# Optimization experiments

Hardware: AMD Instinct MI355X
Metric: run time of the kernel (lower is better)

## Reference

```python
import jax, jax.numpy as jnp
import numpy as np

N_IN, N_HID, N_OUT = 200, 256, 2
BN_EPS = 1e-5


def _mlp(x, W1, b1, W2, b2):
    # two-layer MLP with ELU activations (dropout prob = 0.0 -> omitted)
    h = jax.nn.elu(x @ W1 + b1)
    return jax.nn.elu(h @ W2 + b2)


def _batch_norm(x, gamma, beta):
    # torch BatchNorm1d in training mode over flattened (B*E) rows, biased variance
    m = x.mean(axis=(0, 1))
    v = x.var(axis=(0, 1))
    return (x - m) * jax.lax.rsqrt(v + BN_EPS) * gamma + beta


def setup_inputs() -> dict:
    key = jax.random.key(0)
    ks = jax.random.split(key, 12)
    B, N, T, D = 32, 100, 50, 4
    inputs = jax.random.normal(ks[0], (B, N, T, D), dtype=jnp.float32)
    # one-hot receiver/sender matrices over all N*(N-1) ordered off-diagonal pairs
    idx = np.array([(i, j) for i in range(N) for j in range(N) if i != j])
    eye = np.eye(N, dtype=np.float32)
    rel_rec = jnp.asarray(eye[idx[:, 0]])   # [E, N]
    rel_send = jnp.asarray(eye[idx[:, 1]])  # [E, N]

    def lin(k, fi, fo):  # xavier_normal weight
        std = float(np.sqrt(2.0 / (fi + fo)))
        return jax.random.normal(k, (fi, fo), dtype=jnp.float32) * std

    b = lambda n: jnp.full((n,), 0.1, dtype=jnp.float32)
    return dict(
        inputs=inputs, rel_rec=rel_rec, rel_send=rel_send,
        mlp1_W1=lin(ks[1], N_IN, N_HID), mlp1_b1=b(N_HID),
        mlp1_W2=lin(ks[2], N_HID, N_HID), mlp1_b2=b(N_HID),
        mlp2_W1=lin(ks[3], 2 * N_HID, N_HID), mlp2_b1=b(N_HID),
        mlp2_W2=lin(ks[4], N_HID, N_HID), mlp2_b2=b(N_HID),
        mlp3_W1=lin(ks[5], N_HID, N_HID), mlp3_b1=b(N_HID),
        mlp3_W2=lin(ks[6], N_HID, N_HID), mlp3_b2=b(N_HID),
        mlp4_W1=lin(ks[7], 3 * N_HID, N_HID), mlp4_b1=b(N_HID),
        mlp4_W2=lin(ks[8], N_HID, N_HID), mlp4_b2=b(N_HID),
        mlp4_bn_gamma=jnp.ones((N_HID,), jnp.float32),
        mlp4_bn_beta=jnp.zeros((N_HID,), jnp.float32),
        fc_W=lin(ks[9], N_HID, N_OUT), fc_b=b(N_OUT),
    )


def reference(inputs, rel_rec, rel_send,
              mlp1_W1, mlp1_b1, mlp1_W2, mlp1_b2,
              mlp2_W1, mlp2_b1, mlp2_W2, mlp2_b2,
              mlp3_W1, mlp3_b1, mlp3_W2, mlp3_b2,
              mlp4_W1, mlp4_b1, mlp4_W2, mlp4_b2,
              mlp4_bn_gamma, mlp4_bn_beta, fc_W, fc_b):
    B, N = inputs.shape[0], inputs.shape[1]
    x = inputs.reshape(B, N, -1)                       # [B, N, T*D]
    x = _mlp(x, mlp1_W1, mlp1_b1, mlp1_W2, mlp1_b2)     # [B, N, H]

    def node2edge(h):
        recv = jnp.einsum('en,bnh->beh', rel_rec, h)
        send = jnp.einsum('en,bnh->beh', rel_send, h)
        return jnp.concatenate([send, recv], axis=2)    # [B, E, 2H]

    x = node2edge(x)
    x = _mlp(x, mlp2_W1, mlp2_b1, mlp2_W2, mlp2_b2)     # [B, E, H]
    x_skip = x
    # factor=True branch
    incoming = jnp.einsum('en,beh->bnh', rel_rec, x) / x.shape[1]  # edge2node, /N per code
    x = _mlp(incoming, mlp3_W1, mlp3_b1, mlp3_W2, mlp3_b2)
    x = node2edge(x)                                    # [B, E, 2H]
    x = jnp.concatenate([x, x_skip], axis=2)            # [B, E, 3H]
    x = _mlp(x, mlp4_W1, mlp4_b1, mlp4_W2, mlp4_b2)
    x = _batch_norm(x, mlp4_bn_gamma, mlp4_bn_beta)
    return x @ fc_W + fc_b                              # [B, E, n_out]
```

## Files before the change

### kernel.cpp

```cpp
#include <hip/hip_runtime.h>
#include <math.h>


typedef unsigned short ushort_t;
typedef __bf16 bf16x8 __attribute__((ext_vector_type(8)));
typedef float  f32x4  __attribute__((ext_vector_type(4)));

#define E_EDGES 9900
#define NNODE   100
#define HID     256
#define M_BIG   316800
#define M_SMALL 3200
#define NBLK2   (M_BIG / 128)

__device__ __forceinline__ float bf2f(ushort_t u) {
    union { unsigned int i; float f; } v; v.i = ((unsigned int)u) << 16; return v.f;
}
__device__ __forceinline__ ushort_t f2bf(float f) {
    union { __bf16 h; ushort_t u; } v; v.h = (__bf16)f; return v.u;
}
__device__ __forceinline__ float elu_f(float x) {
    return x > 0.f ? x : (__expf(x) - 1.f);
}

__global__ __launch_bounds__(256)
void wcvt_all(const float* __restrict__ s0, const float* __restrict__ s1,
              const float* __restrict__ s2, const float* __restrict__ s3,
              const float* __restrict__ s4, const float* __restrict__ s5,
              const float* __restrict__ s6, const float* __restrict__ s7,
              ushort_t* d0, ushort_t* d1, ushort_t* d2, ushort_t* d3,
              ushort_t* d4, ushort_t* d5, ushort_t* d6, ushort_t* d7)
{
    int bid = blockIdx.x;
    const float* S; ushort_t* D; int Kd, Kr, t;
    if      (bid < 16)  { S = s0; D = d0; Kd = 256; Kr = 200; t = bid; }
    else if (bid < 32)  { S = s1; D = d1; Kd = 256; Kr = 256; t = bid - 16; }
    else if (bid < 64)  { S = s2; D = d2; Kd = 512; Kr = 512; t = bid - 32; }
    else if (bid < 80)  { S = s3; D = d3; Kd = 256; Kr = 256; t = bid - 64; }
    else if (bid < 96)  { S = s4; D = d4; Kd = 256; Kr = 256; t = bid - 80; }
    else if (bid < 112) { S = s5; D = d5; Kd = 256; Kr = 256; t = bid - 96; }
    else if (bid < 160) { S = s6; D = d6; Kd = 768; Kr = 768; t = bid - 112; }
    else                { S = s7; D = d7; Kd = 256; Kr = 256; t = bid - 160; }
    int k0 = (t >> 2) * 64, c0 = (t & 3) * 64;
    __shared__ float Sh[64][65];
    int tid = threadIdx.x;
    #pragma unroll
    for (int i = 0; i < 16; ++i) {
        int idx = tid + i * 256;
        int kk = idx >> 6, cc = idx & 63;
        Sh[kk][cc] = (k0 + kk < Kr) ? S[(size_t)(k0 + kk) * 256 + c0 + cc] : 0.f;
    }
    __syncthreads();
    int col = tid & 63;
    int kb  = (tid >> 6) * 16;
    ushort_t* dst = D + (size_t)(c0 + col) * Kd + k0 + kb;
    #pragma unroll
    for (int jj = 0; jj < 4; ++jj) {
        ushort4 u;
        u.x = f2bf(Sh[kb + 4 * jj + 0][col]);
        u.y = f2bf(Sh[kb + 4 * jj + 1][col]);
        u.z = f2bf(Sh[kb + 4 * jj + 2][col]);
        u.w = f2bf(Sh[kb + 4 * jj + 3][col]);
        *(ushort4*)(dst + 4 * jj) = u;
    }
}

__device__ __forceinline__ void gemm32(const ushort_t S[32][264],
                                       const ushort_t* __restrict__ WT,
                                       int wstr, int kcn,
                                       int w, int ln15, int klane,
                                       f32x4 acc[2][4])
{
    #pragma unroll
    for (int r = 0; r < 2; ++r)
        #pragma unroll
        for (int c = 0; c < 4; ++c)
            acc[r][c][0] = acc[r][c][1] = acc[r][c][2] = acc[r][c][3] = 0.f;
    int wch[4];
    #pragma unroll
    for (int c = 0; c < 4; ++c) wch[c] = (w * 64 + 16 * c + ln15) * wstr;
    bf16x8 wf0[4];
    #pragma unroll
    for (int c = 0; c < 4; ++c)
        wf0[c] = *(const bf16x8*)(WT + wch[c] + klane);
    for (int kc = 0; kc < kcn; ++kc) {
        bf16x8 wf1[4];
        if (kc + 1 < kcn) {
            #pragma unroll
            for (int c = 0; c < 4; ++c)
                wf1[c] = *(const bf16x8*)(WT + wch[c] + (kc + 1) * 32 + klane);
        }
        bf16x8 af[2];
        #pragma unroll
        for (int r = 0; r < 2; ++r)
            af[r] = *(const bf16x8*)&S[16 * r + ln15][kc * 32 + klane];
        #pragma unroll
        for (int r = 0; r < 2; ++r)
            #pragma unroll
            for (int c = 0; c < 4; ++c)
                acc[r][c] = __builtin_amdgcn_mfma_f32_16x16x32_bf16(wf0[c], af[r], acc[r][c], 0, 0, 0);
        #pragma unroll
        for (int c = 0; c < 4; ++c) wf0[c] = wf1[c];
    }
}

__device__ __forceinline__ void park32(ushort_t D[32][264], f32x4 acc[2][4],
                                       const float* __restrict__ bias,
                                       int act, int w, int ln15, int q)
{
    #pragma unroll
    for (int c = 0; c < 4; ++c) {
        float4 bv = bias ? *(const float4*)&bias[w * 64 + 16 * c + 4 * q]
                         : make_float4(0.f, 0.f, 0.f, 0.f);
        #pragma unroll
        for (int r = 0; r < 2; ++r) {
            float o0 = acc[r][c][0] + bv.x;
            float o1 = acc[r][c][1] + bv.y;
            float o2 = acc[r][c][2] + bv.z;
            float o3 = acc[r][c][3] + bv.w;
            if (act) { o0 = elu_f(o0); o1 = elu_f(o1); o2 = elu_f(o2); o3 = elu_f(o3); }
            ushort4 u;
            u.x = f2bf(o0); u.y = f2bf(o1); u.z = f2bf(o2); u.w = f2bf(o3);
            *(ushort4*)&D[16 * r + ln15][w * 64 + 16 * c + 4 * q] = u;
        }
    }
}

__global__ __launch_bounds__(256, 4)
void mlp_pq(const float* __restrict__ Xf, const float* __restrict__ Xf2,
            int Kreal, int kcN, float xscale,
            const ushort_t* __restrict__ W1T, const float* __restrict__ b1,
            const ushort_t* __restrict__ W2T, const float* __restrict__ b2,
            const ushort_t* __restrict__ WPT, int wsPQ,
            const float* __restrict__ bP, ushort_t* __restrict__ Pout,
            const ushort_t* __restrict__ WQT, ushort_t* __restrict__ Qout)
{
    __shared__ ushort_t Abuf[32][264];
    __shared__ ushort_t Bbuf[32][264];
    const int tid = threadIdx.x;
    const int w = tid >> 6;
    const int l = tid & 63;
    const int ln15 = l & 15;
    const int q = l >> 4;
    const int klane = 8 * q;
    const int Rbase = blockIdx.x * 32;

    {
        int row = tid >> 3, seg = tid & 7;
        if (seg < kcN) {
            ushort_t tmp[32];
            const float* src  = Xf + (size_t)(Rbase + row) * Kreal + seg * 32;
            const float* src2 = Xf2 ? Xf2 + (size_t)(Rbase + row) * Kreal + seg * 32
                                    : (const float*)nullptr;
            #pragma unroll
            for (int u = 0; u < 32; ++u) {
                float a = 0.f;
                if (seg * 32 + u < Kreal) {
                    a = src[u];
                    if (Xf2) a += src2[u];
                }
                tmp[u] = f2bf(a * xscale);
            }
            #pragma unroll
            for (int u = 0; u < 4; ++u)
                *(uint4*)&Abuf[row][seg * 32 + u * 8] = *(uint4*)&tmp[u * 8];
        }
    }
    __syncthreads();

    f32x4 acc[2][4];
    gemm32(Abuf, W1T, 256, kcN, w, ln15, klane, acc);
    park32(Bbuf, acc, b1, 1, w, ln15, q);
    __syncthreads();
    gemm32(Bbuf, W2T, 256, 8, w, ln15, klane, acc);
    park32(Abuf, acc, b2, 1, w, ln15, q);
    __syncthreads();
    gemm32(Abuf, WPT, wsPQ, 8, w, ln15, klane, acc);
    park32(Bbuf, acc, bP, 0, w, ln15, q);
    __syncthreads();
    f32x4 acq[2][4];
    gemm32(Abuf, WQT, wsPQ, 8, w, ln15, klane, acq);
    #pragma unroll
    for (int m = 0; m < 4; ++m) {
        int ch = tid + m * 256;
        int row = ch >> 5;
        int o = (ch & 31) * 8;
        *(uint4*)&Pout[(size_t)(Rbase + row) * 256 + o] = *(const uint4*)&Bbuf[row][o];
    }
    __syncthreads();
    park32(Bbuf, acq, nullptr, 0, w, ln15, q);
    __syncthreads();
    #pragma unroll
    for (int m = 0; m < 4; ++m) {
        int ch = tid + m * 256;
        int row = ch >> 5;
        int o = (ch & 31) * 8;
        *(uint4*)&Qout[(size_t)(Rbase + row) * 256 + o] = *(const uint4*)&Bbuf[row][o];
    }
}

__device__ __forceinline__ void gemm128cs(const ushort_t As[128][264],
                                          const ushort_t* __restrict__ WT,
                                          int wstr, int w, int ln15, int klane,
                                          f32x4 acc[8][2])
{
    #pragma unroll
    for (int r = 0; r < 8; ++r)
        #pragma unroll
        for (int c = 0; c < 2; ++c)
            acc[r][c][0] = acc[r][c][1] = acc[r][c][2] = acc[r][c][3] = 0.f;
    int wch[2];
    #pragma unroll
    for (int c = 0; c < 2; ++c) wch[c] = (w * 32 + 16 * c + ln15) * wstr;
    bf16x8 wf0[2];
    #pragma unroll
    for (int c = 0; c < 2; ++c)
        wf0[c] = *(const bf16x8*)(WT + wch[c] + klane);
    #pragma unroll
    for (int kc = 0; kc < 8; ++kc) {
        bf16x8 wf1[2];
        if (kc < 7) {
            #pragma unroll
            for (int c = 0; c < 2; ++c)
                wf1[c] = *(const bf16x8*)(WT + wch[c] + (kc + 1) * 32 + klane);
        }
        #pragma unroll
        for (int g = 0; g < 2; ++g) {
            bf16x8 af[4];
            #pragma unroll
            for (int r = 0; r < 4; ++r)
                af[r] = *(const bf16x8*)&As[16 * (4 * g + r) + ln15][kc * 32 + klane];
            #pragma unroll
            for (int r = 0; r < 4; ++r)
                #pragma unroll
                for (int c = 0; c < 2; ++c)
                    acc[4 * g + r][c] = __builtin_amdgcn_mfma_f32_16x16x32_bf16(wf0[c], af[r], acc[4 * g + r][c], 0, 0, 0);
        }
        #pragma unroll
        for (int c = 0; c < 2; ++c) wf0[c] = wf1[c];
    }
}

__global__ __launch_bounds__(512, 4)
void edge_mlp2(const ushort_t* __restrict__ Pb, const ushort_t* __restrict__ Qb,
               const ushort_t* __restrict__ W2T,
               const float* __restrict__ b2,
               ushort_t* __restrict__ Y,
               float* __restrict__ part0, float* __restrict__ part1)
{
    __shared__ ushort_t As[128][264];
    const int tid = threadIdx.x;
    const int w = tid >> 6;
    const int l = tid & 63;
    const int ln15 = l & 15;
    const int q = l >> 4;
    const int klane = 8 * q;
    const int Rbase = blockIdx.x * 128;

    {
        int row = tid >> 2;
        int R = Rbase + row;
        int b = R / E_EDGES;
        int e = R - b * E_EDGES;
        int i = e / 99;
        int k = e - 99 * i;
        int j = k + (k >= i ? 1 : 0);
        const ushort_t* prow = Pb + (size_t)(b * NNODE + j) * HID;
        const ushort_t* qrow = Qb + (size_t)(b * NNODE + i) * HID;
        int off = (tid & 3) * 8;
        uint4 pv[8], qv[8];
        #pragma unroll
        for (int u = 0; u < 8; ++u) {
            int o = off + u * 32;
            pv[u] = *(const uint4*)(prow + o);
            qv[u] = *(const uint4*)(qrow + o);
        }
        #pragma unroll
        for (int u = 0; u < 8; ++u) {
            int o = off + u * 32;
            union { uint4 v; ushort_t s[8]; } pu, qu, hu;
            pu.v = pv[u]; qu.v = qv[u];
            #pragma unroll
            for (int x = 0; x < 8; ++x)
                hu.s[x] = f2bf(elu_f(bf2f(pu.s[x]) + bf2f(qu.s[x])));
            *(uint4*)&As[row][o] = hu.v;
        }
    }
    __syncthreads();

    f32x4 acc[8][2];
    gemm128cs(As, W2T, 256, w, ln15, klane, acc);
    __syncthreads();

    #pragma unroll
    for (int c = 0; c < 2; ++c) {
        float4 bv = *(const float4*)&b2[w * 32 + 16 * c + 4 * q];
        #pragma unroll
        for (int r = 0; r < 8; ++r) {
            ushort4 u;
            u.x = f2bf(elu_f(acc[r][c][0] + bv.x));
            u.y = f2bf(elu_f(acc[r][c][1] + bv.y));
            u.z = f2bf(elu_f(acc[r][c][2] + bv.z));
            u.w = f2bf(elu_f(acc[r][c][3] + bv.w));
            *(ushort4*)&As[16 * r + ln15][w * 32 + 16 * c + 4 * q] = u;
        }
    }
    __syncthreads();

    #pragma unroll
    for (int m = 0; m < 8; ++m) {
        int ch = tid + m * 512;
        int row = ch >> 5;
        int o = (ch & 31) * 8;
        *(uint4*)&Y[((size_t)(Rbase + row)) * 256 + o] = *(const uint4*)&As[row][o];
    }

    if (tid < 64) {
        int c4 = tid * 4;
        int bn = Rbase / 99;
        int off0 = Rbase - bn * 99;
        int left = 99 - off0;
        int first = 1;
        float s[4] = {0.f, 0.f, 0.f, 0.f};
        for (int r = 0; r < 128; ++r) {
            union { ushort4 v; ushort_t e4[4]; } u;
            u.v = *(const ushort4*)&As[r][c4];
            #pragma unroll
            for (int g = 0; g < 4; ++g) s[g] += bf2f(u.e4[g]);
            if (--left == 0) {
                float* dst = (first && off0 != 0) ? part1 : part0;
                #pragma unroll
                for (int g = 0; g < 4; ++g) {
                    dst[(size_t)bn * 256 + c4 + g] = s[g];
                    s[g] = 0.f;
                }
                ++bn; left = 99; first = 0;
            }
        }
        if (left != 99) {
            float* dst = (first && off0 != 0) ? part1 : part0;
            #pragma unroll
            for (int g = 0; g < 4; ++g)
                dst[(size_t)bn * 256 + c4 + g] = s[g];
        }
    }
}

__global__ __launch_bounds__(512, 4)
void edge_mlp4(const ushort_t* __restrict__ Pb, const ushort_t* __restrict__ Qb,
               const ushort_t* __restrict__ X2,
               const ushort_t* __restrict__ WaT, int wsA,
               const ushort_t* __restrict__ WbT, int wsB,
               const float* __restrict__ b2,
               ushort_t* __restrict__ Y, ushort_t* __restrict__ pstat)
{
    __shared__ ushort_t As[128][264];
    __shared__ float Sc[4][512];
    const int tid = threadIdx.x;
    const int w = tid >> 6;
    const int l = tid & 63;
    const int ln15 = l & 15;
    const int q = l >> 4;
    const int klane = 8 * q;
    const int Rbase = blockIdx.x * 128;

    {
        int row = tid >> 2;
        const ushort_t* xrow = X2 + (size_t)(Rbase + row) * 256;
        int off = (tid & 3) * 8;
        uint4 xv[8];
        #pragma unroll
        for (int u = 0; u < 8; ++u) xv[u] = *(const uint4*)(xrow + off + u * 32);
        #pragma unroll
        for (int u = 0; u < 8; ++u) *(uint4*)&As[row][off + u * 32] = xv[u];
    }

    int oP[8], oQ[8];
    #pragma unroll
    for (int r = 0; r < 8; ++r) {
        int R = Rbase + 16 * r + ln15;
        int b = R / E_EDGES;
        int e = R - b * E_EDGES;
        int i = e / 99;
        int k = e - 99 * i;
        int j = k + (k >= i ? 1 : 0);
        oP[r] = (b * NNODE + j) * HID;
        oQ[r] = (b * NNODE + i) * HID;
    }
    __syncthreads();

    f32x4 acc[8][2];
    gemm128cs(As, WaT, wsA, w, ln15, klane, acc);
    __syncthreads();

    #pragma unroll
    for (int c = 0; c < 2; ++c) {
        int ch = w * 32 + 16 * c + 4 * q;
        ushort4 pv[8], qv[8];
        #pragma unroll
        for (int r = 0; r < 8; ++r) {
            pv[r] = *(const ushort4*)(Pb + oP[r] + ch);
            qv[r] = *(const ushort4*)(Qb + oQ[r] + ch);
        }
        #pragma unroll
        for (int r = 0; r < 8; ++r) {
            union { ushort4 v; ushort_t s[4]; } pu, qu;
            pu.v = pv[r]; qu.v = qv[r];
            ushort4 u;
            u.x = f2bf(elu_f(acc[r][c][0] + bf2f(pu.s[0]) + bf2f(qu.s[0])));
            u.y = f2bf(elu_f(acc[r][c][1] + bf2f(pu.s[1]) + bf2f(qu.s[1])));
            u.z = f2bf(elu_f(acc[r][c][2] + bf2f(pu.s[2]) + bf2f(qu.s[2])));
            u.w = f2bf(elu_f(acc[r][c][3] + bf2f(pu.s[3]) + bf2f(qu.s[3])));
            *(ushort4*)&As[16 * r + ln15][ch] = u;
        }
    }
    __syncthreads();

    gemm128cs(As, WbT, wsB, w, ln15, klane, acc);
    __syncthreads();

    #pragma unroll
    for (int c = 0; c < 2; ++c) {
        float4 bv = *(const float4*)&b2[w * 32 + 16 * c + 4 * q];
        #pragma unroll
        for (int r = 0; r < 8; ++r) {
            ushort4 u;
            u.x = f2bf(elu_f(acc[r][c][0] + bv.x));
            u.y = f2bf(elu_f(acc[r][c][1] + bv.y));
            u.z = f2bf(elu_f(acc[r][c][2] + bv.z));
            u.w = f2bf(elu_f(acc[r][c][3] + bv.w));
            *(ushort4*)&As[16 * r + ln15][w * 32 + 16 * c + 4 * q] = u;
        }
    }
    __syncthreads();

    #pragma unroll
    for (int m = 0; m < 8; ++m) {
        int ch = tid + m * 512;
        int row = ch >> 5;
        int o = (ch & 31) * 8;
        *(uint4*)&Y[((size_t)(Rbase + row)) * 256 + o] = *(const uint4*)&As[row][o];
    }

    if (w < 4) {
        int c4 = l * 4;
        float s[4] = {0.f, 0.f, 0.f, 0.f};
        float qq[4] = {0.f, 0.f, 0.f, 0.f};
        for (int r = w * 32; r < w * 32 + 32; ++r) {
            union { ushort4 v; ushort_t e4[4]; } u;
            u.v = *(const ushort4*)&As[r][c4];
            #pragma unroll
            for (int g = 0; g < 4; ++g) {
                float v = bf2f(u.e4[g]);
                s[g] += v;
                qq[g] = fmaf(v, v, qq[g]);
            }
        }
        #pragma unroll
        for (int g = 0; g < 4; ++g) {
            Sc[w][c4 + g]       = s[g];
            Sc[w][256 + c4 + g] = qq[g];
        }
    }
    __syncthreads();
    {
        float v = Sc[0][tid] + Sc[1][tid] + Sc[2][tid] + Sc[3][tid];
        pstat[(size_t)blockIdx.x * 512 + tid] = f2bf(v);
    }
}

__global__ __launch_bounds__(256)
void reduce_stats(const ushort_t* __restrict__ pstat, float* __restrict__ stats)
{
    int c = threadIdx.x;
    float s = 0.f, q = 0.f;
    for (int b = blockIdx.x; b < NBLK2; b += 64) {
        size_t base = (size_t)b * 512;
        s += bf2f(pstat[base + c]);
        q += bf2f(pstat[base + 256 + c]);
    }
    atomicAdd(&stats[c], s);
    atomicAdd(&stats[256 + c], q);
}

__global__ __launch_bounds__(256)
void fold_kernel(const float* __restrict__ stats,
                 const float* __restrict__ gamma, const float* __restrict__ beta,
                 const float* __restrict__ fcW, const float* __restrict__ fcb,
                 float* __restrict__ fold)
{
    __shared__ float red0[256], red1[256];
    int c = threadIdx.x;
    float mean  = stats[c] * (1.f / M_BIG);
    float var   = stats[256 + c] * (1.f / M_BIG) - mean * mean;
    float inv   = rsqrtf(var + 1e-5f);
    float scale = inv * gamma[c];
    float sh    = beta[c] - mean * scale;
    float w0 = fcW[c * 2 + 0], w1 = fcW[c * 2 + 1];
    fold[c * 2 + 0] = scale * w0;
    fold[c * 2 + 1] = scale * w1;
    red0[c] = sh * w0;
    red1[c] = sh * w1;
    __syncthreads();
    for (int off = 128; off > 0; off >>= 1) {
        if (c < off) { red0[c] += red0[c + off]; red1[c] += red1[c + off]; }
        __syncthreads();
    }
    if (c == 0) {
        fold[512] = red0[0] + fcb[0];
        fold[513] = red1[0] + fcb[1];
    }
}

__global__ __launch_bounds__(256)
void final_kernel(const ushort_t* __restrict__ x4, const float* __restrict__ fold,
                  float* __restrict__ out)
{
    int tid  = threadIdx.x;
    int l32  = tid & 31;
    int g    = tid >> 5;
    int R = blockIdx.x * 8 + g;
    int c0 = l32 * 8;
    union { uint4 qv; ushort_t s[8]; } u;
    u.qv = *(const uint4*)(x4 + (size_t)R * 256 + c0);
    float a0 = 0.f, a1 = 0.f;
    #pragma unroll
    for (int j = 0; j < 8; ++j) {
        float v = bf2f(u.s[j]);
        a0 = fmaf(v, fold[(c0 + j) * 2 + 0], a0);
        a1 = fmaf(v, fold[(c0 + j) * 2 + 1], a1);
    }
    #pragma unroll
    for (int off = 16; off > 0; off >>= 1) {
        a0 += __shfl_down(a0, off);
        a1 += __shfl_down(a1, off);
    }
    if (l32 == 0) {
        out[(size_t)R * 2 + 0] = a0 + fold[512];
        out[(size_t)R * 2 + 1] = a1 + fold[513];
    }
}

extern "C" void kernel_launch(void* const* d_in, const int* in_sizes, int n_in,
                              void* d_out, int out_size, void* d_ws, size_t ws_size,
                              hipStream_t stream)
{
    (void)in_sizes; (void)n_in; (void)out_size; (void)ws_size;

    const float* inputs = (const float*)d_in[0];
    const float* m1W1 = (const float*)d_in[3];
    const float* m1b1 = (const float*)d_in[4];
    const float* m1W2 = (const float*)d_in[5];
    const float* m1b2 = (const float*)d_in[6];
    const float* m2W1 = (const float*)d_in[7];
    const float* m2b1 = (const float*)d_in[8];
    const float* m2W2 = (const float*)d_in[9];
    const float* m2b2 = (const float*)d_in[10];
    const float* m3W1 = (const float*)d_in[11];
    const float* m3b1 = (const float*)d_in[12];
    const float* m3W2 = (const float*)d_in[13];
    const float* m3b2 = (const float*)d_in[14];
    const float* m4W1 = (const float*)d_in[15];
    const float* m4b1 = (const float*)d_in[16];
    const float* m4W2 = (const float*)d_in[17];
    const float* m4b2 = (const float*)d_in[18];
    const float* gamma = (const float*)d_in[19];
    const float* beta  = (const float*)d_in[20];
    const float* fcW   = (const float*)d_in[21];
    const float* fcb   = (const float*)d_in[22];
    float* out = (float*)d_out;

    char* ws = (char*)d_ws;
    const size_t BIGB = (size_t)M_BIG * 256 * 2;
    const size_t HB   = (size_t)M_SMALL * 256 * 2;
    const size_t SM4  = (size_t)M_SMALL * 256 * 4;
    ushort_t* bigX     = (ushort_t*)ws;
    ushort_t* pstat    = (ushort_t*)(ws + BIGB);
    float*    part1    = (float*)(ws + BIGB);
    float*    part0    = (float*)(ws + BIGB + 2 * HB);
    ushort_t* Pbuf     = (ushort_t*)(ws + BIGB + 2 * HB + SM4);
    ushort_t* Qbuf     = (ushort_t*)(ws + BIGB + 3 * HB + SM4);
    float*    stats    = (float*)(ws + BIGB + 4 * HB + SM4);
    float*    fold     = stats + 512;
    ushort_t* w1t      = (ushort_t*)(ws + BIGB + 4 * HB + SM4 + 8192);
    ushort_t* w1bt     = w1t  + 256 * 256;
    ushort_t* w2pt     = w1bt + 256 * 256;
    ushort_t* w2t      = w2pt + 256 * 512;
    ushort_t* w3at     = w2t  + 256 * 256;
    ushort_t* w3bt     = w3at + 256 * 256;
    ushort_t* w4pt     = w3bt + 256 * 256;
    ushort_t* w4bt     = w4pt + 256 * 768;

    hipMemsetAsync(stats, 0, 2048, stream);
    hipMemsetAsync(part1, 0, SM4, stream);

    dim3 blk(256);
    dim3 blk512(512);
    wcvt_all<<<176, blk, 0, stream>>>(m1W1, m1W2, m2W1, m2W2, m3W1, m3W2, m4W1, m4W2,
                                      w1t, w1bt, w2pt, w2t, w3at, w3bt, w4pt, w4bt);
    mlp_pq<<<100, blk, 0, stream>>>(inputs, nullptr, 200, 7, 1.f,
                                    w1t, m1b1, w1bt, m1b2,
                                    w2pt, 512, m2b1, Pbuf,
                                    w2pt + 256, Qbuf);
    edge_mlp2<<<NBLK2, blk512, 0, stream>>>(Pbuf, Qbuf, w2t, m2b2, bigX, part0, part1);
    mlp_pq<<<100, blk, 0, stream>>>(part0, part1, 256, 8, 1.f / 9900.f,
                                    w3at, m3b1, w3bt, m3b2,
                                    w4pt, 768, m4b1, Pbuf,
                                    w4pt + 256, Qbuf);
    edge_mlp4<<<NBLK2, blk512, 0, stream>>>(Pbuf, Qbuf, bigX,
                                            w4pt + 512, 768, w4bt, 256,
                                            m4b2, bigX, pstat);
    reduce_stats<<<64, blk, 0, stream>>>(pstat, stats);
    fold_kernel<<<1, blk, 0, stream>>>(stats, gamma, beta, fcW, fcb, fold);
    final_kernel<<<M_BIG / 8, blk, 0, stream>>>(bigX, fold, out);
}
```

Before: 471.5 us.

## Fuse column stats into GEMM epilogue and prefetch weights and gathers before barriers

Per-column sums (edge2node partial sums and batch-norm sum/sumsq) are now accumulated in registers during the ELU epilogue and reduced with wave shuffles. This replaces the serial LDS re-read done by a subset of threads and removes a shared scratch buffer and a barrier. Each GEMM's first weight fragment and the P/Q gather loads are also issued before the preceding barrier, so global latency overlaps with LDS work. The cost is higher register pressure, and the stats are summed from fp32 values instead of bf16-rounded ones, which slightly changes numerics.

```diff
diff --git a/kernel.cpp b/kernel.cpp
--- a/kernel.cpp
+++ b/kernel.cpp
@@ -199,10 +199,19 @@
     }
 }
 
+__device__ __forceinline__ void wf0_load(const ushort_t* __restrict__ WT,
+                                         int wstr, int w, int ln15, int klane,
+                                         bf16x8 wf0[2])
+{
+    #pragma unroll
+    for (int c = 0; c < 2; ++c)
+        wf0[c] = *(const bf16x8*)(WT + (w * 32 + 16 * c + ln15) * wstr + klane);
+}
+
 __device__ __forceinline__ void gemm128cs(const ushort_t As[128][264],
                                           const ushort_t* __restrict__ WT,
                                           int wstr, int w, int ln15, int klane,
-                                          f32x4 acc[8][2])
+                                          bf16x8 wf0[2], f32x4 acc[8][2])
 {
     #pragma unroll
     for (int r = 0; r < 8; ++r)
@@ -212,10 +221,6 @@
     int wch[2];
     #pragma unroll
     for (int c = 0; c < 2; ++c) wch[c] = (w * 32 + 16 * c + ln15) * wstr;
-    bf16x8 wf0[2];
-    #pragma unroll
-    for (int c = 0; c < 2; ++c)
-        wf0[c] = *(const bf16x8*)(WT + wch[c] + klane);
     #pragma unroll
     for (int kc = 0; kc < 8; ++kc) {
         bf16x8 wf1[2];
@@ -286,23 +291,56 @@
             *(uint4*)&As[row][o] = hu.v;
         }
     }
+    bf16x8 wf0[2];
+    wf0_load(W2T, 256, w, ln15, klane, wf0);
     __syncthreads();
 
     f32x4 acc[8][2];
-    gemm128cs(As, W2T, 256, w, ln15, klane, acc);
-    __syncthreads();
+    gemm128cs(As, W2T, 256, w, ln15, klane, wf0, acc);
+    __syncthreads();
+
+    const int g0   = Rbase / 99;
+    const int off0 = Rbase - g0 * 99;
+    const int t1   = 99 - off0;
+    const int t2   = t1 + 99;
+    float sA[8], sB[8], sC[8];
+    #pragma unroll
+    for (int j = 0; j < 8; ++j) { sA[j] = sB[j] = sC[j] = 0.f; }
 
     #pragma unroll
     for (int c = 0; c < 2; ++c) {
         float4 bv = *(const float4*)&b2[w * 32 + 16 * c + 4 * q];
         #pragma unroll
         for (int r = 0; r < 8; ++r) {
+            int row = 16 * r + ln15;
+            float o0 = elu_f(acc[r][c][0] + bv.x);
+            float o1 = elu_f(acc[r][c][1] + bv.y);
+            float o2 = elu_f(acc[r][c][2] + bv.z);
+            float o3 = elu_f(acc[r][c][3] + bv.w);
+            sA[c * 4 + 0] += o0; sA[c * 4 + 1] += o1;
+            sA[c * 4 + 2] += o2; sA[c * 4 + 3] += o3;
+            float m1 = (row >= t1) ? 1.f : 0.f;
+            float m2 = (row >= t2) ? 1.f : 0.f;
+            sB[c * 4 + 0] = fmaf(m1, o0, sB[c * 4 + 0]);
+            sB[c * 4 + 1] = fmaf(m1, o1, sB[c * 4 + 1]);
+            sB[c * 4 + 2] = fmaf(m1, o2, sB[c * 4 + 2]);
+            sB[c * 4 + 3] = fmaf(m1, o3, sB[c * 4 + 3]);
+            sC[c * 4 + 0] = fmaf(m2, o0, sC[c * 4 + 0]);
+            sC[c * 4 + 1] = fmaf(m2, o1, sC[c * 4 + 1]);
+            sC[c * 4 + 2] = fmaf(m2, o2, sC[c * 4 + 2]);
+            sC[c * 4 + 3] = fmaf(m2, o3, sC[c * 4 + 3]);
             ushort4 u;
-            u.x = f2bf(elu_f(acc[r][c][0] + bv.x));
-            u.y = f2bf(elu_f(acc[r][c][1] + bv.y));
-            u.z = f2bf(elu_f(acc[r][c][2] + bv.z));
-            u.w = f2bf(elu_f(acc[r][c][3] + bv.w));
-            *(ushort4*)&As[16 * r + ln15][w * 32 + 16 * c + 4 * q] = u;
+            u.x = f2bf(o0); u.y = f2bf(o1); u.z = f2bf(o2); u.w = f2bf(o3);
+            *(ushort4*)&As[row][w * 32 + 16 * c + 4 * q] = u;
+        }
+    }
+    #pragma unroll
+    for (int m = 1; m <= 8; m <<= 1) {
+        #pragma unroll
+        for (int j = 0; j < 8; ++j) {
+            sA[j] += __shfl_xor(sA[j], m);
+            sB[j] += __shfl_xor(sB[j], m);
+            sC[j] += __shfl_xor(sC[j], m);
         }
     }
     __syncthreads();
@@ -315,33 +353,26 @@
         *(uint4*)&Y[((size_t)(Rbase + row)) * 256 + o] = *(const uint4*)&As[row][o];
     }
 
-    if (tid < 64) {
-        int c4 = tid * 4;
-        int bn = Rbase / 99;
-        int off0 = Rbase - bn * 99;
-        int left = 99 - off0;
-        int first = 1;
-        float s[4] = {0.f, 0.f, 0.f, 0.f};
-        for (int r = 0; r < 128; ++r) {
-            union { ushort4 v; ushort_t e4[4]; } u;
-            u.v = *(const ushort4*)&As[r][c4];
-            #pragma unroll
-            for (int g = 0; g < 4; ++g) s[g] += bf2f(u.e4[g]);
-            if (--left == 0) {
-                float* dst = (first && off0 != 0) ? part1 : part0;
-                #pragma unroll
-                for (int g = 0; g < 4; ++g) {
-                    dst[(size_t)bn * 256 + c4 + g] = s[g];
-                    s[g] = 0.f;
-                }
-                ++bn; left = 99; first = 0;
-            }
-        }
-        if (left != 99) {
-            float* dst = (first && off0 != 0) ? part1 : part0;
-            #pragma unroll
-            for (int g = 0; g < 4; ++g)
-                dst[(size_t)bn * 256 + c4 + g] = s[g];
+    if (ln15 == 0) {
+        float* d0 = (off0 != 0) ? part1 : part0;
+        #pragma unroll
+        for (int c = 0; c < 2; ++c) {
+            int col = w * 32 + 16 * c + 4 * q;
+            float4 v0, v1, v2;
+            v0.x = sA[c * 4 + 0] - sB[c * 4 + 0];
+            v0.y = sA[c * 4 + 1] - sB[c * 4 + 1];
+            v0.z = sA[c * 4 + 2] - sB[c * 4 + 2];
+            v0.w = sA[c * 4 + 3] - sB[c * 4 + 3];
+            v1.x = sB[c * 4 + 0] - sC[c * 4 + 0];
+            v1.y = sB[c * 4 + 1] - sC[c * 4 + 1];
+            v1.z = sB[c * 4 + 2] - sC[c * 4 + 2];
+            v1.w = sB[c * 4 + 3] - sC[c * 4 + 3];
+            v2.x = sC[c * 4 + 0]; v2.y = sC[c * 4 + 1];
+            v2.z = sC[c * 4 + 2]; v2.w = sC[c * 4 + 3];
+            *(float4*)&d0[(size_t)g0 * 256 + col] = v0;
+            *(float4*)&part0[(size_t)(g0 + 1) * 256 + col] = v1;
+            if (t2 < 128)
+                *(float4*)&part0[(size_t)(g0 + 2) * 256 + col] = v2;
         }
     }
 }
@@ -355,7 +386,6 @@
                ushort_t* __restrict__ Y, ushort_t* __restrict__ pstat)
 {
     __shared__ ushort_t As[128][264];
-    __shared__ float Sc[4][512];
     const int tid = threadIdx.x;
     const int w = tid >> 6;
     const int l = tid & 63;
@@ -387,49 +417,87 @@
         oP[r] = (b * NNODE + j) * HID;
         oQ[r] = (b * NNODE + i) * HID;
     }
+
+    const int ch0 = w * 32 + 4 * q;
+    ushort4 pv0[8], qv0[8];
+    #pragma unroll
+    for (int r = 0; r < 8; ++r) {
+        pv0[r] = *(const ushort4*)(Pb + oP[r] + ch0);
+        qv0[r] = *(const ushort4*)(Qb + oQ[r] + ch0);
+    }
+    bf16x8 wfa[2];
+    wf0_load(WaT, wsA, w, ln15, klane, wfa);
     __syncthreads();
 
     f32x4 acc[8][2];
-    gemm128cs(As, WaT, wsA, w, ln15, klane, acc);
-    __syncthreads();
-
-    #pragma unroll
-    for (int c = 0; c < 2; ++c) {
-        int ch = w * 32 + 16 * c + 4 * q;
-        ushort4 pv[8], qv[8];
-        #pragma unroll
-        for (int r = 0; r < 8; ++r) {
-            pv[r] = *(const ushort4*)(Pb + oP[r] + ch);
-            qv[r] = *(const ushort4*)(Qb + oQ[r] + ch);
-        }
-        #pragma unroll
-        for (int r = 0; r < 8; ++r) {
-            union { ushort4 v; ushort_t s[4]; } pu, qu;
-            pu.v = pv[r]; qu.v = qv[r];
-            ushort4 u;
-            u.x = f2bf(elu_f(acc[r][c][0] + bf2f(pu.s[0]) + bf2f(qu.s[0])));
-            u.y = f2bf(elu_f(acc[r][c][1] + bf2f(pu.s[1]) + bf2f(qu.s[1])));
-            u.z = f2bf(elu_f(acc[r][c][2] + bf2f(pu.s[2]) + bf2f(qu.s[2])));
-            u.w = f2bf(elu_f(acc[r][c][3] + bf2f(pu.s[3]) + bf2f(qu.s[3])));
-            *(ushort4*)&As[16 * r + ln15][ch] = u;
-        }
-    }
-    __syncthreads();
-
-    gemm128cs(As, WbT, wsB, w, ln15, klane, acc);
-    __syncthreads();
-
+    gemm128cs(As, WaT, wsA, w, ln15, klane, wfa, acc);
+    bf16x8 wfb[2];
+    wf0_load(WbT, wsB, w, ln15, klane, wfb);
+    __syncthreads();
+
+    const int ch1 = ch0 + 16;
+    ushort4 pv1[8], qv1[8];
+    #pragma unroll
+    for (int r = 0; r < 8; ++r) {
+        pv1[r] = *(const ushort4*)(Pb + oP[r] + ch1);
+        qv1[r] = *(const ushort4*)(Qb + oQ[r] + ch1);
+    }
+    #pragma unroll
+    for (int r = 0; r < 8; ++r) {
+        union { ushort4 v; ushort_t s[4]; } pu, qu;
+        pu.v = pv0[r]; qu.v = qv0[r];
+        ushort4 u;
+        u.x = f2bf(elu_f(acc[r][0][0] + bf2f(pu.s[0]) + bf2f(qu.s[0])));
+        u.y = f2bf(elu_f(acc[r][0][1] + bf2f(pu.s[1]) + bf2f(qu.s[1])));
+        u.z = f2bf(elu_f(acc[r][0][2] + bf2f(pu.s[2]) + bf2f(qu.s[2])));
+        u.w = f2bf(elu_f(acc[r][0][3] + bf2f(pu.s[3]) + bf2f(qu.s[3])));
+        *(ushort4*)&As[16 * r + ln15][ch0] = u;
+    }
+    #pragma unroll
+    for (int r = 0; r < 8; ++r) {
+        union { ushort4 v; ushort_t s[4]; } pu, qu;
+        pu.v = pv1[r]; qu.v = qv1[r];
+        ushort4 u;
+        u.x = f2bf(elu_f(acc[r][1][0] + bf2f(pu.s[0]) + bf2f(qu.s[0])));
+        u.y = f2bf(elu_f(acc[r][1][1] + bf2f(pu.s[1]) + bf2f(qu.s[1])));
+        u.z = f2bf(elu_f(acc[r][1][2] + bf2f(pu.s[2]) + bf2f(qu.s[2])));
+        u.w = f2bf(elu_f(acc[r][1][3] + bf2f(pu.s[3]) + bf2f(qu.s[3])));
+        *(ushort4*)&As[16 * r + ln15][ch1] = u;
+    }
+    __syncthreads();
+
+    gemm128cs(As, WbT, wsB, w, ln15, klane, wfb, acc);
+    __syncthreads();
+
+    float sS[8], sQ[8];
+    #pragma unroll
+    for (int j = 0; j < 8; ++j) { sS[j] = sQ[j] = 0.f; }
     #pragma unroll
     for (int c = 0; c < 2; ++c) {
         float4 bv = *(const float4*)&b2[w * 32 + 16 * c + 4 * q];
         #pragma unroll
         for (int r = 0; r < 8; ++r) {
+            float o0 = elu_f(acc[r][c][0] + bv.x);
+            float o1 = elu_f(acc[r][c][1] + bv.y);
+            float o2 = elu_f(acc[r][c][2] + bv.z);
+            float o3 = elu_f(acc[r][c][3] + bv.w);
+            sS[c * 4 + 0] += o0; sS[c * 4 + 1] += o1;
+            sS[c * 4 + 2] += o2; sS[c * 4 + 3] += o3;
+            sQ[c * 4 + 0] = fmaf(o0, o0, sQ[c * 4 + 0]);
+            sQ[c * 4 + 1] = fmaf(o1, o1, sQ[c * 4 + 1]);
+            sQ[c * 4 + 2] = fmaf(o2, o2, sQ[c * 4 + 2]);
+            sQ[c * 4 + 3] = fmaf(o3, o3, sQ[c * 4 + 3]);
             ushort4 u;
-            u.x = f2bf(elu_f(acc[r][c][0] + bv.x));
-            u.y = f2bf(elu_f(acc[r][c][1] + bv.y));
-            u.z = f2bf(elu_f(acc[r][c][2] + bv.z));
-            u.w = f2bf(elu_f(acc[r][c][3] + bv.w));
+            u.x = f2bf(o0); u.y = f2bf(o1); u.z = f2bf(o2); u.w = f2bf(o3);
             *(ushort4*)&As[16 * r + ln15][w * 32 + 16 * c + 4 * q] = u;
+        }
+    }
+    #pragma unroll
+    for (int m = 1; m <= 8; m <<= 1) {
+        #pragma unroll
+        for (int j = 0; j < 8; ++j) {
+            sS[j] += __shfl_xor(sS[j], m);
+            sQ[j] += __shfl_xor(sQ[j], m);
         }
     }
     __syncthreads();
@@ -442,30 +510,18 @@
         *(uint4*)&Y[((size_t)(Rbase + row)) * 256 + o] = *(const uint4*)&As[row][o];
     }
 
-    if (w < 4) {
-        int c4 = l * 4;
-        float s[4] = {0.f, 0.f, 0.f, 0.f};
-        float qq[4] = {0.f, 0.f, 0.f, 0.f};
-        for (int r = w * 32; r < w * 32 + 32; ++r) {
-            union { ushort4 v; ushort_t e4[4]; } u;
-            u.v = *(const ushort4*)&As[r][c4];
-            #pragma unroll
-            for (int g = 0; g < 4; ++g) {
-                float v = bf2f(u.e4[g]);
-                s[g] += v;
-                qq[g] = fmaf(v, v, qq[g]);
-            }
-        }
-        #pragma unroll
-        for (int g = 0; g < 4; ++g) {
-            Sc[w][c4 + g]       = s[g];
-            Sc[w][256 + c4 + g] = qq[g];
-        }
-    }
-    __syncthreads();
-    {
-        float v = Sc[0][tid] + Sc[1][tid] + Sc[2][tid] + Sc[3][tid];
-        pstat[(size_t)blockIdx.x * 512 + tid] = f2bf(v);
+    if (ln15 == 0) {
+        #pragma unroll
+        for (int c = 0; c < 2; ++c) {
+            int col = w * 32 + 16 * c + 4 * q;
+            ushort4 us, uq;
+            us.x = f2bf(sS[c * 4 + 0]); us.y = f2bf(sS[c * 4 + 1]);
+            us.z = f2bf(sS[c * 4 + 2]); us.w = f2bf(sS[c * 4 + 3]);
+            uq.x = f2bf(sQ[c * 4 + 0]); uq.y = f2bf(sQ[c * 4 + 1]);
+            uq.z = f2bf(sQ[c * 4 + 2]); uq.w = f2bf(sQ[c * 4 + 3]);
+            *(ushort4*)&pstat[(size_t)blockIdx.x * 512 + col]       = us;
+            *(ushort4*)&pstat[(size_t)blockIdx.x * 512 + 256 + col] = uq;
+        }
     }
 }
 
```

Result: slower. 490.2 us (+4.0%).
